# Performance work log

Measured on AMD Instinct MI355X. Metric: run time of the kernel, lower is better.

## Reference

```python
import math
import jax, jax.numpy as jnp
import numpy as np

B, N, DIM, E, G, TOPK, DEPTH = 64, 512, 128, 16, 32, 4, 1
HID = 4 * DIM
EPS = 1e-8
LAMBDA_INIT = 0.8 - 0.6 * math.exp(-0.3 * DEPTH)


def setup_inputs() -> dict:
    key = jax.random.key(0)
    ks = jax.random.split(key, 16)
    d = {}
    d["x"] = jax.random.normal(ks[0], (B, N, DIM), jnp.float32)
    d["bias"] = jnp.zeros((1,), jnp.float32)
    d["attn_scale"] = jnp.ones((DIM,), jnp.float32)
    d["ffn_scale"] = jnp.ones((DIM,), jnp.float32)
    d["Wr"] = jax.random.normal(ks[1], (DIM, E), jnp.float32) * 0.05
    d["br"] = jnp.zeros((E,), jnp.float32)
    d["E1"] = jax.random.uniform(ks[2], (2, E, N, G), jnp.float32)
    d["E2"] = jax.random.uniform(ks[3], (2, E, G, N), jnp.float32)
    d["lambda_q1"] = jax.random.normal(ks[4], (DIM,), jnp.float32) * 0.1
    d["lambda_k1"] = jax.random.normal(ks[5], (DIM,), jnp.float32) * 0.1
    d["lambda_q2"] = jax.random.normal(ks[6], (DIM,), jnp.float32) * 0.1
    d["lambda_k2"] = jax.random.normal(ks[7], (DIM,), jnp.float32) * 0.1
    d["outer_lambda"] = jnp.log(jnp.asarray(99.0, jnp.float32))
    d["W1"] = jax.random.normal(ks[8], (DIM, HID), jnp.float32) * 0.02
    d["b1"] = jnp.zeros((HID,), jnp.float32)
    d["W2"] = jax.random.normal(ks[9], (DIM, HID), jnp.float32) * 0.02
    d["b2"] = jnp.zeros((HID,), jnp.float32)
    d["W3"] = jax.random.normal(ks[10], (HID, DIM), jnp.float32) * 0.02
    d["b3"] = jnp.zeros((DIM,), jnp.float32)
    return d


def _rmsnorm(v, scale):
    # RMSNorm with p<0: full L2 norm over last dim, rms = ||v|| / sqrt(d)
    rms = jnp.linalg.norm(v, axis=-1, keepdims=True) * (DIM ** -0.5)
    return scale * (v / (rms + EPS))


def reference(x, bias, attn_scale, ffn_scale, Wr, br, E1, E2,
              lambda_q1, lambda_k1, lambda_q2, lambda_k2, outer_lambda,
              W1, b1, W2, b2, W3, b3):
    # ---- pre-norm ----
    xn = _rmsnorm(x, attn_scale)                       # [B,N,F]

    # ---- top-k routing (selector) ----
    route_logits = xn @ Wr + br                        # [B,N,E]
    gate = jax.nn.sigmoid(route_logits)
    _, topk_idx = jax.lax.top_k(gate + bias, TOPK)     # [B,N,K]
    mask = jnp.sum(jax.nn.one_hot(topk_idx, E, dtype=gate.dtype), axis=-2)  # [B,N,E]
    # sigmoid(route + log(mask)) == sigmoid(route) * mask (mask in {0,1})
    gated = gate * mask
    route = gated / jnp.sum(gated, axis=-1, keepdims=True)

    # ---- coefficient: concat([1], -(exp(q1.k1) - exp(q2.k2) + lambda_init)) ----
    l1 = jnp.exp(jnp.sum(lambda_q1 * lambda_k1))
    l2 = jnp.exp(jnp.sum(lambda_q2 * lambda_k2))
    lambda_full = -(l1 - l2 + LAMBDA_INIT)
    coef = jnp.concatenate([jnp.ones((1,), x.dtype), lambda_full[None]])  # [2]

    # ---- outer mixing matrix (convex comb of eye with itself -> eye, kept faithful) ----
    w = jax.nn.sigmoid(outer_lambda)
    eye = jnp.eye(DIM, dtype=x.dtype)
    outer = w * eye + (1.0 - w) * eye                  # [F,F]

    # ---- expert graph mixing: bik,e,ekid,ekdj,bjf,fc->bic ----
    A1 = jax.nn.softmax(E1, axis=-1)                   # [2,E,N,G]
    A2 = jax.nn.softmax(E2, axis=-1)                   # [2,E,G,N]
    M = jnp.einsum('ekid,ekdj->ekij', A1, A2)          # [2,E,N,N]
    s = jnp.einsum('bik,ekij->beij', route, M)         # [B,2,N,N]
    xc = jnp.einsum('bjf,fc->bjc', xn, outer)          # [B,N,F]
    attn = jnp.einsum('e,beij,bjc->bic', coef, s, xc)  # [B,N,F]

    x = x + attn

    # ---- SwiGLU FFN (dropout is identity at inference) ----
    xn2 = _rmsnorm(x, ffn_scale)
    h = jax.nn.silu(xn2 @ W1 + b1) * (xn2 @ W2 + b2)   # [B,N,4F]
    x = x + h @ W3 + b3
    return x, topk_idx
```

## Files before the change

### kernel.cpp

```cpp
#include <hip/hip_runtime.h>
#include <math.h>

#define B_ 64
#define N_ 512
#define DIM_ 128
#define E_ 16
#define G_ 32
#define TOPK_ 4
#define HID_ 512

constexpr int BN_ROWS = B_ * N_;

using bf16x8 = __attribute__((ext_vector_type(8))) short;
using s16x4  = __attribute__((ext_vector_type(4))) short;
using f32x4  = __attribute__((ext_vector_type(4))) float;

__device__ __forceinline__ float bf2f(short s) {
    union { unsigned u; float f; } x;
    x.u = ((unsigned)(unsigned short)s) << 16;
    return x.f;
}
__device__ __forceinline__ short f2bf(float f) {
    union { float f; unsigned u; } x;
    x.f = f;
    unsigned r = x.u + 0x7FFF + ((x.u >> 16) & 1);
    return (short)(r >> 16);
}

__device__ __forceinline__ bf16x8 frag_ld(const short* base, int row, int ks, int lhi) {
    int addr = row * 128 + (((ks * 64) + lhi * 16) ^ ((row & 7) << 4));
    return *(const bf16x8*)((const char*)base + addr);
}
__device__ __forceinline__ bf16x8 frag_ld128(const short* base, int row, int ks, int lhi) {
    int addr = row * 256 + (((ks * 64) + lhi * 16) ^ ((row & 7) << 4));
    return *(const bf16x8*)((const char*)base + addr);
}

typedef __attribute__((address_space(3))) void lds_vt;
typedef __attribute__((address_space(1))) const void gbl_vt;
__device__ __forceinline__ void gl2lds(const void* g, void* l) {
    __builtin_amdgcn_global_load_lds((gbl_vt*)g, (lds_vt*)l, 16, 0, 0);
}
#define WAIT_VMCNT(N) do { asm volatile("s_waitcnt vmcnt(" #N ")" ::: "memory"); \
    __builtin_amdgcn_sched_barrier(0); } while (0)
__device__ __forceinline__ void barrier_() {
    __builtin_amdgcn_sched_barrier(0);
    __builtin_amdgcn_s_barrier();
    __builtin_amdgcn_sched_barrier(0);
}
__device__ __forceinline__ void lgkm0_bar() {
    asm volatile("s_waitcnt lgkmcnt(0)" ::: "memory");
    __builtin_amdgcn_sched_barrier(0);
    __builtin_amdgcn_s_barrier();
    __builtin_amdgcn_sched_barrier(0);
}

constexpr int NPRE = BN_ROWS / 4;
constexpr int NXNT = B_ * 16;
constexpr int NSMG = 32 * 512 / 8;
constexpr int NSMN = 1024 / 4;
constexpr int NTW  = 64 * 3;
constexpr int NMISC = NPRE + NXNT + NSMG + NSMN + NTW + 1;

__global__ __launch_bounds__(256) void k_misc(
    const float* __restrict__ x, const float* __restrict__ attn_s,
    const float* __restrict__ Wr, const float* __restrict__ br, const float* __restrict__ bias,
    float* __restrict__ route, float* __restrict__ topk_out,
    short* __restrict__ xnT,
    const float* __restrict__ E1, short* __restrict__ A1nb,
    const float* __restrict__ E2, short* __restrict__ A2nb,
    const float* __restrict__ W1, const float* __restrict__ W2, const float* __restrict__ W3,
    short* __restrict__ W1T, short* __restrict__ W2T, short* __restrict__ W3T,
    const float* __restrict__ lq1, const float* __restrict__ lk1,
    const float* __restrict__ lq2, const float* __restrict__ lk2,
    float lam_init, float* __restrict__ lam_out) {
    __shared__ float tb[32][129];
    __shared__ float invb[32];
    __shared__ float tw[32][33];
    int blk = blockIdx.x;
    int tid = threadIdx.x;

    if (blk < NPRE) {
        int w = tid >> 6, lane = tid & 63;
        int row = blk * 4 + w;
        float2 v = ((const float2*)(x + (size_t)row * DIM_))[lane];
        float ss = v.x * v.x + v.y * v.y;
        for (int off = 32; off; off >>= 1) ss += __shfl_xor(ss, off);
        float inv = 1.0f / (sqrtf(ss * (1.0f / DIM_)) + 1e-8f);
        float2 s = ((const float2*)attn_s)[lane];
        float xn0 = v.x * inv * s.x;
        float xn1 = v.y * inv * s.y;
        int e = lane & 15, chunk = lane >> 4;
        float acc = 0.f;
#pragma unroll
        for (int j = 0; j < 16; ++j) {
            int srcl = chunk * 16 + j;
            float a0 = __shfl(xn0, srcl);
            float a1 = __shfl(xn1, srcl);
            int d0 = chunk * 32 + 2 * j;
            acc += a0 * Wr[d0 * E_ + e] + a1 * Wr[(d0 + 1) * E_ + e];
        }
        acc += __shfl_xor(acc, 16);
        acc += __shfl_xor(acc, 32);
        float gate = 1.0f / (1.0f + expf(-(acc + br[e])));
        float vv = gate + bias[0];
        int rank = 0;
#pragma unroll
        for (int i = 0; i < 16; ++i) {
            float vi = __shfl(vv, i);
            rank += ((vi > vv) || (vi == vv && i < e)) ? 1 : 0;
        }
        bool selq = (rank < TOPK_) && (lane < 16);
        float contrib = selq ? gate : 0.f;
        float ssum = contrib;
        ssum += __shfl_xor(ssum, 1); ssum += __shfl_xor(ssum, 2);
        ssum += __shfl_xor(ssum, 4); ssum += __shfl_xor(ssum, 8);
        if (lane < 16) route[(size_t)row * E_ + e] = selq ? gate / ssum : 0.0f;
        if (selq) topk_out[(size_t)row * TOPK_ + rank] = (float)e;
        return;
    }
    blk -= NPRE;

    if (blk < NXNT) {
        int b = blk >> 4, j0 = (blk & 15) * 32;
        const float* src = x + (size_t)(b * 512 + j0) * 128;
        int r = tid >> 3, c8 = tid & 7;
#pragma unroll
        for (int it = 0; it < 4; ++it) {
            int c4 = c8 + it * 8;
            float4 w4 = *(const float4*)(src + (size_t)r * 128 + c4 * 4);
            tb[r][c4 * 4 + 0] = w4.x; tb[r][c4 * 4 + 1] = w4.y;
            tb[r][c4 * 4 + 2] = w4.z; tb[r][c4 * 4 + 3] = w4.w;
        }
        __syncthreads();
        int sg = tid & 7;
        float ps = 0.f;
#pragma unroll
        for (int j = 0; j < 16; ++j) { float e2 = tb[r][sg * 16 + j]; ps += e2 * e2; }
        ps += __shfl_xor(ps, 1); ps += __shfl_xor(ps, 2); ps += __shfl_xor(ps, 4);
        if (sg == 0) invb[r] = 1.0f / (sqrtf(ps * (1.0f / DIM_)) + 1e-8f);
        __syncthreads();
        int c = tid >> 1, half = tid & 1;
        float sc = attn_s[c];
        short ov[16];
#pragma unroll
        for (int j = 0; j < 16; ++j) {
            int jj = half * 16 + j;
            ov[j] = f2bf(tb[jj][c] * invb[jj] * sc);
        }
        short* dst = xnT + (size_t)(b * 128 + c) * 512 + j0 + half * 16;
        *(bf16x8*)dst = *(bf16x8*)ov;
        *(bf16x8*)(dst + 8) = *(bf16x8*)(ov + 8);
        return;
    }
    blk -= NXNT;

    if (blk < NSMG) {
        int row = blk * 8 + (tid >> 5);
        int l = tid & 31;
        float v = E1[(size_t)row * 32 + l];
        float m = v;
        for (int off = 16; off; off >>= 1) m = fmaxf(m, __shfl_xor(m, off));
        float ev = expf(v - m);
        float s = ev;
        for (int off = 16; off; off >>= 1) s += __shfl_xor(s, off);
        A1nb[(size_t)row * 32 + l] = f2bf(ev / s);
        return;
    }
    blk -= NSMG;

    if (blk < NSMN) {
        int row = blk * 4 + (tid >> 6);
        int l = tid & 63;
        const float* p = E2 + (size_t)row * 512;
        float v[8];
        float m = -1e30f;
#pragma unroll
        for (int j = 0; j < 8; ++j) { v[j] = p[l + j * 64]; m = fmaxf(m, v[j]); }
        for (int off = 32; off; off >>= 1) m = fmaxf(m, __shfl_xor(m, off));
        float s = 0.f;
#pragma unroll
        for (int j = 0; j < 8; ++j) { v[j] = expf(v[j] - m); s += v[j]; }
        for (int off = 32; off; off >>= 1) s += __shfl_xor(s, off);
        float inv = 1.0f / s;
        short* q = A2nb + (size_t)row * 512;
#pragma unroll
        for (int j = 0; j < 8; ++j) q[l + j * 64] = f2bf(v[j] * inv);
        return;
    }
    blk -= NSMN;

    if (blk < NTW) {
        int m = blk >> 6, tile = blk & 63;
        const float* S = (m == 0) ? W1 : (m == 1) ? W2 : W3;
        short* D = (m == 0) ? W1T : (m == 1) ? W2T : W3T;
        int R = (m == 2) ? 512 : 128, C = (m == 2) ? 128 : 512;
        int ctiles = C / 32;
        int r0 = (tile / ctiles) * 32, c0 = (tile % ctiles) * 32;
        int tx = tid & 31, ty = tid >> 5;
#pragma unroll
        for (int r = 0; r < 4; ++r) tw[ty * 4 + r][tx] = S[(size_t)(r0 + ty * 4 + r) * C + c0 + tx];
        __syncthreads();
#pragma unroll
        for (int r = 0; r < 4; ++r) D[(size_t)(c0 + ty * 4 + r) * R + r0 + tx] = f2bf(tw[tx][ty * 4 + r]);
        return;
    }

    if (tid < 64) {
        int l = tid;
        float s1 = lq1[l] * lk1[l] + lq1[l + 64] * lk1[l + 64];
        float s2 = lq2[l] * lk2[l] + lq2[l + 64] * lk2[l + 64];
        for (int off = 32; off; off >>= 1) {
            s1 += __shfl_xor(s1, off);
            s2 += __shfl_xor(s2, off);
        }
        if (l == 0) lam_out[0] = -(expf(s1) - expf(s2) + lam_init);
    }
}

__global__ __launch_bounds__(256) void k_gemm_y(const short* __restrict__ A2nb,
                                                const short* __restrict__ xnT,
                                                short* __restrict__ YT) {
    alignas(16) __shared__ short As0[128 * 64];
    alignas(16) __shared__ short Bs0[128 * 64];
    alignas(16) __shared__ short As1[128 * 64];
    alignas(16) __shared__ short Bs1[128 * 64];
    int id = blockIdx.x;
    int nid = ((id & 7) << 6) + (id >> 3);
    int m0 = (nid & 3) * 128;
    int be = nid >> 2, b = be >> 1, e = be & 1;
    int tid = threadIdx.x, lane = tid & 63, wid = tid >> 6;
    int l15 = lane & 15, lhi = lane >> 4;
    int wr = wid >> 1, wc = wid & 1;
    const short* Asrc = A2nb + (size_t)e * 512 * 512 + (size_t)m0 * 512;
    const short* Bsrc = xnT + (size_t)b * 128 * 512;
    int row8 = lane >> 3;
    int chunk8 = (lane & 7) ^ row8;

    auto stage = [&](short* Ad, short* Bd, int k0) {
#pragma unroll
        for (int t = 0; t < 4; ++t) {
            int i = wid * 4 + t;
            int row = i * 8 + row8;
            gl2lds(Asrc + (size_t)row * 512 + k0 + chunk8 * 8, (char*)Ad + i * 1024);
            gl2lds(Bsrc + (size_t)row * 512 + k0 + chunk8 * 8, (char*)Bd + i * 1024);
        }
    };
    f32x4 acc[4][4] = {};
    stage(As0, Bs0, 0);
    for (int s = 0; s < 8; ++s) {
        const short* Ac = (s & 1) ? As1 : As0;
        const short* Bc = (s & 1) ? Bs1 : Bs0;
        if (s < 7) {
            stage((s & 1) ? As0 : As1, (s & 1) ? Bs0 : Bs1, (s + 1) * 64);
            WAIT_VMCNT(8);
        } else {
            WAIT_VMCNT(0);
        }
        barrier_();
#pragma unroll
        for (int ks = 0; ks < 2; ++ks) {
            bf16x8 af[4], bfr[4];
#pragma unroll
            for (int i = 0; i < 4; ++i) af[i] = frag_ld(Ac, wr * 64 + i * 16 + l15, ks, lhi);
#pragma unroll
            for (int j = 0; j < 4; ++j) bfr[j] = frag_ld(Bc, wc * 64 + j * 16 + l15, ks, lhi);
#pragma unroll
            for (int i = 0; i < 4; ++i)
#pragma unroll
                for (int j = 0; j < 4; ++j)
                    acc[i][j] = __builtin_amdgcn_mfma_f32_16x16x32_bf16(af[i], bfr[j], acc[i][j], 0, 0, 0);
        }
        barrier_();
    }
    short* Yb = YT + (size_t)b * 128 * 1024 + e * 512;
#pragma unroll
    for (int i = 0; i < 4; ++i) {
        int mbase = m0 + wr * 64 + i * 16 + lhi * 4;
#pragma unroll
        for (int j = 0; j < 4; ++j) {
            int n = wc * 64 + j * 16 + l15;
            s16x4 o;
#pragma unroll
            for (int q = 0; q < 4; ++q) o[q] = f2bf(acc[i][j][q]);
            *(s16x4*)(Yb + (size_t)n * 1024 + mbase) = o;
        }
    }
}

__global__ __launch_bounds__(256) void k_attn(const short* __restrict__ A1nb,
                                              const float* __restrict__ route,
                                              const short* __restrict__ YT,
                                              const float* __restrict__ x,
                                              const float* __restrict__ lam_p,
                                              const float* __restrict__ ffn_s,
                                              float* __restrict__ x1,
                                              short* __restrict__ xn2b) {
    alignas(16) __shared__ short Ab0[64 * 64];
    alignas(16) __shared__ short Ab1[64 * 64];
    alignas(16) __shared__ short Bb0[128 * 64];
    alignas(16) __shared__ short Bb1[128 * 64];
    __shared__ float ssbuf[2][64];
    int id = blockIdx.x;
    int nid = ((id & 7) << 6) + (id >> 3);
    int m0 = (nid & 7) * 64;
    int b = nid >> 3;
    float lam = lam_p[0];
    int tid = threadIdx.x, lane = tid & 63, wid = tid >> 6;
    int l15 = lane & 15, lhi = lane >> 4;
    int wr = wid >> 1, wc = wid & 1;
    const short* YTb = YT + (size_t)b * 128 * 1024;
    int row8 = lane >> 3;
    int chunk8 = (lane & 7) ^ row8;

    auto stageB = [&](short* Bd, int k0) {
#pragma unroll
        for (int t = 0; t < 4; ++t) {
            int i = wid * 4 + t;
            int row = i * 8 + row8;
            gl2lds(YTb + (size_t)row * 1024 + k0 + chunk8 * 8, (char*)Bd + i * 1024);
        }
    };
    auto loadA = [&](float (&rv)[2], bf16x8 (&ar)[2], int sn) {
#pragma unroll
        for (int r = 0; r < 2; ++r) {
            int idx = tid + r * 256, rowl = idx >> 3, slot = idx & 7;
            int t = sn * 2 + (slot >> 2);
            int gi = m0 + rowl;
            rv[r] = route[((size_t)b * 512 + gi) * 16 + (t & 15)] * (t >= 16 ? lam : 1.0f);
            ar[r] = *(const bf16x8*)(A1nb + ((size_t)t * 512 + gi) * 32 + (slot & 3) * 8);
        }
    };
    auto writeA = [&](short* dst, float (&rv)[2], bf16x8 (&ar)[2]) {
#pragma unroll
        for (int r = 0; r < 2; ++r) {
            int idx = tid + r * 256, rowl = idx >> 3, slot = idx & 7;
            bf16x8 o;
#pragma unroll
            for (int q = 0; q < 8; ++q) o[q] = f2bf(bf2f(ar[r][q]) * rv[r]);
            *(bf16x8*)((char*)dst + rowl * 128 + ((slot * 16) ^ ((rowl & 7) << 4))) = o;
        }
    };
    f32x4 acc[2][4] = {};
    auto compute = [&](const short* Ac, const short* Bc) {
#pragma unroll
        for (int ks = 0; ks < 2; ++ks) {
            bf16x8 af[2], bfr[4];
#pragma unroll
            for (int i = 0; i < 2; ++i) af[i] = frag_ld(Ac, wr * 32 + i * 16 + l15, ks, lhi);
#pragma unroll
            for (int j = 0; j < 4; ++j) bfr[j] = frag_ld(Bc, wc * 64 + j * 16 + l15, ks, lhi);
#pragma unroll
            for (int i = 0; i < 2; ++i)
#pragma unroll
                for (int j = 0; j < 4; ++j)
                    acc[i][j] = __builtin_amdgcn_mfma_f32_16x16x32_bf16(af[i], bfr[j], acc[i][j], 0, 0, 0);
        }
    };

    float rv0[2], rv1[2];
    bf16x8 ar0[2], ar1[2];
    stageB(Bb0, 0);
    loadA(rv0, ar0, 0);
    for (int sp = 0; sp < 8; ++sp) {
        int s = sp * 2;
        stageB(Bb1, (s + 1) * 64);
        loadA(rv1, ar1, s + 1);
        WAIT_VMCNT(8);
        barrier_();
        writeA(Ab0, rv0, ar0);
        lgkm0_bar();
        compute(Ab0, Bb0);
        barrier_();
        if (s + 2 < 16) {
            stageB(Bb0, (s + 2) * 64);
            loadA(rv0, ar0, s + 2);
            WAIT_VMCNT(8);
        } else {
            WAIT_VMCNT(0);
        }
        barrier_();
        writeA(Ab1, rv1, ar1);
        lgkm0_bar();
        compute(Ab1, Bb1);
        barrier_();
    }
    float x1v[2][4][4];
    float pss[2][4] = {};
#pragma unroll
    for (int i = 0; i < 2; ++i) {
        int gibase = m0 + wr * 32 + i * 16 + lhi * 4;
#pragma unroll
        for (int j = 0; j < 4; ++j) {
            int n = wc * 64 + j * 16 + l15;
#pragma unroll
            for (int q = 0; q < 4; ++q) {
                size_t off = ((size_t)b * 512 + gibase + q) * 128 + n;
                float val = acc[i][j][q] + x[off];
                x1[off] = val;
                x1v[i][j][q] = val;
                pss[i][q] += val * val;
            }
        }
    }
#pragma unroll
    for (int i = 0; i < 2; ++i)
#pragma unroll
        for (int q = 0; q < 4; ++q) {
            float p = pss[i][q];
            p += __shfl_xor(p, 1); p += __shfl_xor(p, 2);
            p += __shfl_xor(p, 4); p += __shfl_xor(p, 8);
            pss[i][q] = p;
        }
    if (l15 == 0) {
#pragma unroll
        for (int i = 0; i < 2; ++i)
#pragma unroll
            for (int q = 0; q < 4; ++q)
                ssbuf[wc][wr * 32 + i * 16 + lhi * 4 + q] = pss[i][q];
    }
    __syncthreads();
#pragma unroll
    for (int i = 0; i < 2; ++i)
#pragma unroll
        for (int q = 0; q < 4; ++q) {
            int rowl = wr * 32 + i * 16 + lhi * 4 + q;
            float ssum = ssbuf[0][rowl] + ssbuf[1][rowl];
            float inv = 1.0f / (sqrtf(ssum * (1.0f / DIM_)) + 1e-8f);
#pragma unroll
            for (int j = 0; j < 4; ++j) {
                int n = wc * 64 + j * 16 + l15;
                xn2b[((size_t)b * 512 + m0 + rowl) * 128 + n] = f2bf(x1v[i][j][q] * inv * ffn_s[n]);
            }
        }
}

__global__ __launch_bounds__(256) void k_ffn(const short* __restrict__ xn2b,
                                             const short* __restrict__ W1T, const float* __restrict__ b1,
                                             const short* __restrict__ W2T, const float* __restrict__ b2,
                                             const short* __restrict__ W3T, const float* __restrict__ b3,
                                             const float* __restrict__ x1,
                                             float* __restrict__ out) {
    alignas(16) __shared__ short Xs[64 * 128];
    alignas(16) __shared__ short Hs[64 * 64];
    alignas(16) __shared__ short W1s[64 * 128];
    alignas(16) __shared__ short W2s[64 * 128];
    alignas(16) __shared__ short W3s[128 * 64];
    int id = blockIdx.x;
    int nid = ((id & 7) << 6) + (id >> 3);
    int m0 = nid * 64;
    int tid = threadIdx.x, lane = tid & 63, wid = tid >> 6;
    int l15 = lane & 15, lhi = lane >> 4;
    int wr = wid >> 1, wc = wid & 1;

    int r4 = lane >> 4;
    int c16 = lane & 15;
    int r8 = lane >> 3;
    int c8 = lane & 7;

    auto stageX = [&]() {
#pragma unroll
        for (int t = 0; t < 4; ++t) {
            int i = wid * 4 + t;
            int row = i * 4 + r4;
            int cs = c16 ^ (row & 7);
            gl2lds(xn2b + (size_t)(m0 + row) * 128 + cs * 8, (char*)Xs + i * 1024);
        }
    };
    auto stageW12 = [&](int p) {
        int n0 = p * 64;
#pragma unroll
        for (int t = 0; t < 8; ++t) {
            int i = wid * 8 + t;
            int which = i >> 4;
            int ii = i & 15;
            int row = ii * 4 + r4;
            int cs = c16 ^ (row & 7);
            const short* S = which ? W2T : W1T;
            short* D = which ? (short*)W2s : (short*)W1s;
            gl2lds(S + (size_t)(n0 + row) * 128 + cs * 8, (char*)D + ii * 1024);
        }
    };
    auto stageW3 = [&](int p) {
        int n0 = p * 64;
#pragma unroll
        for (int t = 0; t < 4; ++t) {
            int i = wid * 4 + t;
            int row = i * 8 + r8;
            int cs = c8 ^ (row & 7);
            gl2lds(W3T + (size_t)row * 512 + n0 + cs * 8, (char*)W3s + i * 1024);
        }
    };

    f32x4 aout[2][4] = {};
    stageX();
    stageW12(0);
    stageW3(0);
    WAIT_VMCNT(0);
    barrier_();
    for (int p = 0; p < 8; ++p) {
        f32x4 a1[2][2] = {}, a2[2][2] = {};
#pragma unroll
        for (int ks = 0; ks < 4; ++ks) {
            bf16x8 af[2], b1f[2], b2f[2];
#pragma unroll
            for (int i = 0; i < 2; ++i) af[i] = frag_ld128(Xs, wr * 32 + i * 16 + l15, ks, lhi);
#pragma unroll
            for (int j = 0; j < 2; ++j) {
                b1f[j] = frag_ld128(W1s, wc * 32 + j * 16 + l15, ks, lhi);
                b2f[j] = frag_ld128(W2s, wc * 32 + j * 16 + l15, ks, lhi);
            }
#pragma unroll
            for (int i = 0; i < 2; ++i)
#pragma unroll
                for (int j = 0; j < 2; ++j) {
                    a1[i][j] = __builtin_amdgcn_mfma_f32_16x16x32_bf16(af[i], b1f[j], a1[i][j], 0, 0, 0);
                    a2[i][j] = __builtin_amdgcn_mfma_f32_16x16x32_bf16(af[i], b2f[j], a2[i][j], 0, 0, 0);
                }
        }
        int nn0 = p * 64;
#pragma unroll
        for (int i = 0; i < 2; ++i) {
            int mloc = wr * 32 + i * 16 + lhi * 4;
#pragma unroll
            for (int j = 0; j < 2; ++j) {
                int nloc = wc * 32 + j * 16 + l15;
                float bb1 = b1[nn0 + nloc], bb2 = b2[nn0 + nloc];
#pragma unroll
                for (int q = 0; q < 4; ++q) {
                    float u = a1[i][j][q] + bb1;
                    float w2v = a2[i][j][q] + bb2;
                    float hv = u / (1.0f + expf(-u)) * w2v;
                    int mq = mloc + q;
                    *(short*)((char*)Hs + mq * 128 + ((nloc * 2) ^ ((mq & 7) << 4))) = f2bf(hv);
                }
            }
        }
        lgkm0_bar();
        if (p < 7) stageW12(p + 1);
#pragma unroll
        for (int ks = 0; ks < 2; ++ks) {
            bf16x8 af[2], bfr[4];
#pragma unroll
            for (int i = 0; i < 2; ++i) af[i] = frag_ld(Hs, wr * 32 + i * 16 + l15, ks, lhi);
#pragma unroll
            for (int j = 0; j < 4; ++j) bfr[j] = frag_ld(W3s, wc * 64 + j * 16 + l15, ks, lhi);
#pragma unroll
            for (int i = 0; i < 2; ++i)
#pragma unroll
                for (int j = 0; j < 4; ++j)
                    aout[i][j] = __builtin_amdgcn_mfma_f32_16x16x32_bf16(af[i], bfr[j], aout[i][j], 0, 0, 0);
        }
        barrier_();
        if (p < 7) {
            stageW3(p + 1);
            WAIT_VMCNT(0);
            barrier_();
        }
    }
#pragma unroll
    for (int i = 0; i < 2; ++i) {
        int mbase = m0 + wr * 32 + i * 16 + lhi * 4;
#pragma unroll
        for (int j = 0; j < 4; ++j) {
            int n = wc * 64 + j * 16 + l15;
            float bv = b3[n];
#pragma unroll
            for (int q = 0; q < 4; ++q) {
                size_t off = (size_t)(mbase + q) * 128 + n;
                out[off] = aout[i][j][q] + x1[off] + bv;
            }
        }
    }
}

constexpr size_t ALIGN_UP(size_t x) { return (x + 255) & ~(size_t)255; }
constexpr size_t SZ_X1   = ALIGN_UP((size_t)BN_ROWS * DIM_ * 4);
constexpr size_t SZ_RT   = ALIGN_UP((size_t)BN_ROWS * E_ * 4);
constexpr size_t SZ_A1   = ALIGN_UP((size_t)32 * 512 * 32 * 2);
constexpr size_t SZ_A2   = ALIGN_UP((size_t)2 * 512 * 512 * 2);
constexpr size_t SZ_XNT  = ALIGN_UP((size_t)B_ * 128 * 512 * 2);
constexpr size_t SZ_YT   = ALIGN_UP((size_t)B_ * 128 * 1024 * 2);
constexpr size_t SZ_XN2B = ALIGN_UP((size_t)BN_ROWS * DIM_ * 2);
constexpr size_t SZ_WT   = ALIGN_UP((size_t)128 * 512 * 2);

extern "C" void kernel_launch(void* const* d_in, const int* in_sizes, int n_in,
                              void* d_out, int out_size, void* d_ws, size_t ws_size,
                              hipStream_t stream) {
    const float* x      = (const float*)d_in[0];
    const float* bias   = (const float*)d_in[1];
    const float* attn_s = (const float*)d_in[2];
    const float* ffn_s  = (const float*)d_in[3];
    const float* Wr     = (const float*)d_in[4];
    const float* br     = (const float*)d_in[5];
    const float* E1     = (const float*)d_in[6];
    const float* E2     = (const float*)d_in[7];
    const float* lq1    = (const float*)d_in[8];
    const float* lk1    = (const float*)d_in[9];
    const float* lq2    = (const float*)d_in[10];
    const float* lk2    = (const float*)d_in[11];
    const float* W1     = (const float*)d_in[13];
    const float* b1     = (const float*)d_in[14];
    const float* W2     = (const float*)d_in[15];
    const float* b2     = (const float*)d_in[16];
    const float* W3     = (const float*)d_in[17];
    const float* b3     = (const float*)d_in[18];

    char* p = (char*)d_ws;
    float* x1   = (float*)p;            p += SZ_X1;
    float* rt   = (float*)p;            p += SZ_RT;
    short* A1nb = (short*)p;            p += SZ_A1;
    short* A2nb = (short*)p;            p += SZ_A2;
    short* xnT  = (short*)p;            p += SZ_XNT;
    short* YT   = (short*)p;            p += SZ_YT;
    short* xn2b = (short*)p;            p += SZ_XN2B;
    short* W1T  = (short*)p;            p += SZ_WT;
    short* W2T  = (short*)p;            p += SZ_WT;
    short* W3T  = (short*)p;            p += SZ_WT;
    float* lam  = (float*)p;            p += 256;

    float* out_x   = (float*)d_out;
    float* out_idx = out_x + (size_t)BN_ROWS * DIM_;

    float lam_init = 0.8f - 0.6f * expf(-0.3f);

    hipLaunchKernelGGL(k_misc, dim3(NMISC), dim3(256), 0, stream,
                       x, attn_s, Wr, br, bias, rt, out_idx, xnT,
                       E1, A1nb, E2, A2nb, W1, W2, W3, W1T, W2T, W3T,
                       lq1, lk1, lq2, lk2, lam_init, lam);
    hipLaunchKernelGGL(k_gemm_y, dim3(512), dim3(256), 0, stream, A2nb, xnT, YT);
    hipLaunchKernelGGL(k_attn, dim3(512), dim3(256), 0, stream, A1nb, rt, YT, x, lam, ffn_s, x1, xn2b);
    hipLaunchKernelGGL(k_ffn, dim3(512), dim3(256), 0, stream, xn2b, W1T, b1, W2T, b2, W3T, b3, x1, out_x);
}
```

Measured before the change: 197.1 us.

## Fuse attention epilogue with SwiGLU FFN and merge routing into transpose blocks

Merges k_attn and k_ffn into one kernel. The residual x1 stays in registers, and the normalized xn2 is written straight into a swizzled LDS tile, so the fp32 x1 and bf16 xn2b global round trips and one launch go away. The routing/top-k computation moves into the xnT transpose blocks, which already hold the x tile in shared memory, so the separate per-row routing blocks and their second read of x are removed. In exchange the fused kernel aliases a 72KB LDS buffer across its phases, which may lower occupancy. It also prefetches W tiles early, before the norm phase.

```diff
diff --git a/kernel.cpp b/kernel.cpp
--- a/kernel.cpp
+++ b/kernel.cpp
@@ -55,12 +55,11 @@
     __builtin_amdgcn_sched_barrier(0);
 }
 
-constexpr int NPRE = BN_ROWS / 4;
 constexpr int NXNT = B_ * 16;
 constexpr int NSMG = 32 * 512 / 8;
 constexpr int NSMN = 1024 / 4;
 constexpr int NTW  = 64 * 3;
-constexpr int NMISC = NPRE + NXNT + NSMG + NSMN + NTW + 1;
+constexpr int NMISC = NXNT + NSMG + NSMN + NTW + 1;
 
 __global__ __launch_bounds__(256) void k_misc(
     const float* __restrict__ x, const float* __restrict__ attn_s,
@@ -74,52 +73,12 @@
     const float* __restrict__ lq1, const float* __restrict__ lk1,
     const float* __restrict__ lq2, const float* __restrict__ lk2,
     float lam_init, float* __restrict__ lam_out) {
-    __shared__ float tb[32][129];
+    __shared__ float tb[32][132];
     __shared__ float invb[32];
+    __shared__ float gbuf[32][17];
     __shared__ float tw[32][33];
     int blk = blockIdx.x;
     int tid = threadIdx.x;
-
-    if (blk < NPRE) {
-        int w = tid >> 6, lane = tid & 63;
-        int row = blk * 4 + w;
-        float2 v = ((const float2*)(x + (size_t)row * DIM_))[lane];
-        float ss = v.x * v.x + v.y * v.y;
-        for (int off = 32; off; off >>= 1) ss += __shfl_xor(ss, off);
-        float inv = 1.0f / (sqrtf(ss * (1.0f / DIM_)) + 1e-8f);
-        float2 s = ((const float2*)attn_s)[lane];
-        float xn0 = v.x * inv * s.x;
-        float xn1 = v.y * inv * s.y;
-        int e = lane & 15, chunk = lane >> 4;
-        float acc = 0.f;
-#pragma unroll
-        for (int j = 0; j < 16; ++j) {
-            int srcl = chunk * 16 + j;
-            float a0 = __shfl(xn0, srcl);
-            float a1 = __shfl(xn1, srcl);
-            int d0 = chunk * 32 + 2 * j;
-            acc += a0 * Wr[d0 * E_ + e] + a1 * Wr[(d0 + 1) * E_ + e];
-        }
-        acc += __shfl_xor(acc, 16);
-        acc += __shfl_xor(acc, 32);
-        float gate = 1.0f / (1.0f + expf(-(acc + br[e])));
-        float vv = gate + bias[0];
-        int rank = 0;
-#pragma unroll
-        for (int i = 0; i < 16; ++i) {
-            float vi = __shfl(vv, i);
-            rank += ((vi > vv) || (vi == vv && i < e)) ? 1 : 0;
-        }
-        bool selq = (rank < TOPK_) && (lane < 16);
-        float contrib = selq ? gate : 0.f;
-        float ssum = contrib;
-        ssum += __shfl_xor(ssum, 1); ssum += __shfl_xor(ssum, 2);
-        ssum += __shfl_xor(ssum, 4); ssum += __shfl_xor(ssum, 8);
-        if (lane < 16) route[(size_t)row * E_ + e] = selq ? gate / ssum : 0.0f;
-        if (selq) topk_out[(size_t)row * TOPK_ + rank] = (float)e;
-        return;
-    }
-    blk -= NPRE;
 
     if (blk < NXNT) {
         int b = blk >> 4, j0 = (blk & 15) * 32;
@@ -140,6 +99,48 @@
         ps += __shfl_xor(ps, 1); ps += __shfl_xor(ps, 2); ps += __shfl_xor(ps, 4);
         if (sg == 0) invb[r] = 1.0f / (sqrtf(ps * (1.0f / DIM_)) + 1e-8f);
         __syncthreads();
+        {
+            int eb = tid & 7;
+            float invr = invb[r];
+            float g0 = 0.f, g1 = 0.f;
+#pragma unroll 4
+            for (int d4 = 0; d4 < 32; ++d4) {
+                float4 tv = *(const float4*)&tb[r][d4 * 4];
+                float4 sv = *(const float4*)(attn_s + d4 * 4);
+                float x0 = tv.x * sv.x, x1v = tv.y * sv.y, x2 = tv.z * sv.z, x3 = tv.w * sv.w;
+                int d0 = d4 * 4;
+                g0 += x0 * Wr[(d0 + 0) * 16 + eb] + x1v * Wr[(d0 + 1) * 16 + eb]
+                    + x2 * Wr[(d0 + 2) * 16 + eb] + x3 * Wr[(d0 + 3) * 16 + eb];
+                g1 += x0 * Wr[(d0 + 0) * 16 + eb + 8] + x1v * Wr[(d0 + 1) * 16 + eb + 8]
+                    + x2 * Wr[(d0 + 2) * 16 + eb + 8] + x3 * Wr[(d0 + 3) * 16 + eb + 8];
+            }
+            float gate0 = 1.0f / (1.0f + expf(-(g0 * invr + br[eb])));
+            float gate1 = 1.0f / (1.0f + expf(-(g1 * invr + br[eb + 8])));
+            gbuf[r][eb] = gate0;
+            gbuf[r][eb + 8] = gate1;
+        }
+        __syncthreads();
+        {
+            int eb = tid & 7;
+            float bv = bias[0];
+            float gate0 = gbuf[r][eb], gate1 = gbuf[r][eb + 8];
+            float v0 = gate0 + bv, v1 = gate1 + bv;
+            int rank0 = 0, rank1 = 0;
+#pragma unroll
+            for (int i = 0; i < 16; ++i) {
+                float vi = gbuf[r][i] + bv;
+                rank0 += ((vi > v0) || (vi == v0 && i < eb)) ? 1 : 0;
+                rank1 += ((vi > v1) || (vi == v1 && i < eb + 8)) ? 1 : 0;
+            }
+            bool s0 = rank0 < TOPK_, s1 = rank1 < TOPK_;
+            float s = (s0 ? gate0 : 0.f) + (s1 ? gate1 : 0.f);
+            s += __shfl_xor(s, 1); s += __shfl_xor(s, 2); s += __shfl_xor(s, 4);
+            size_t grow = (size_t)b * 512 + j0 + r;
+            route[grow * 16 + eb]     = s0 ? gate0 / s : 0.f;
+            route[grow * 16 + eb + 8] = s1 ? gate1 / s : 0.f;
+            if (s0) topk_out[grow * 4 + rank0] = (float)eb;
+            if (s1) topk_out[grow * 4 + rank1] = (float)(eb + 8);
+        }
         int c = tid >> 1, half = tid & 1;
         float sc = attn_s[c];
         short ov[16];
@@ -288,19 +289,26 @@
     }
 }
 
-__global__ __launch_bounds__(256) void k_attn(const short* __restrict__ A1nb,
-                                              const float* __restrict__ route,
-                                              const short* __restrict__ YT,
-                                              const float* __restrict__ x,
-                                              const float* __restrict__ lam_p,
-                                              const float* __restrict__ ffn_s,
-                                              float* __restrict__ x1,
-                                              short* __restrict__ xn2b) {
-    alignas(16) __shared__ short Ab0[64 * 64];
-    alignas(16) __shared__ short Ab1[64 * 64];
-    alignas(16) __shared__ short Bb0[128 * 64];
-    alignas(16) __shared__ short Bb1[128 * 64];
-    __shared__ float ssbuf[2][64];
+__global__ __launch_bounds__(256) void k_attn_ffn(
+    const short* __restrict__ A1nb, const float* __restrict__ route,
+    const short* __restrict__ YT, const float* __restrict__ x,
+    const float* __restrict__ lam_p, const float* __restrict__ ffn_s,
+    const short* __restrict__ W1T, const float* __restrict__ b1,
+    const short* __restrict__ W2T, const float* __restrict__ b2,
+    const short* __restrict__ W3T, const float* __restrict__ b3,
+    float* __restrict__ out) {
+    alignas(16) __shared__ char L[73728];
+    short* Xs    = (short*)L;
+    short* Hs    = (short*)(L + 16384);
+    float* ssbuf = (float*)(L + 16384);
+    short* W1s   = (short*)(L + 24576);
+    short* W2s   = (short*)(L + 40960);
+    short* W3s   = (short*)(L + 57344);
+    short* Ab0 = (short*)(L + 16384);
+    short* Ab1 = (short*)(L + 24576);
+    short* Bb0 = (short*)(L + 32768);
+    short* Bb1 = (short*)(L + 49152);
+
     int id = blockIdx.x;
     int nid = ((id & 7) << 6) + (id >> 3);
     int m0 = (nid & 7) * 64;
@@ -312,6 +320,7 @@
     const short* YTb = YT + (size_t)b * 128 * 1024;
     int row8 = lane >> 3;
     int chunk8 = (lane & 7) ^ row8;
+    int r4 = lane >> 4, c16 = lane & 15;
 
     auto stageB = [&](short* Bd, int k0) {
 #pragma unroll
@@ -385,6 +394,33 @@
         compute(Ab1, Bb1);
         barrier_();
     }
+
+    auto stageW12 = [&](int p) {
+        int n0 = p * 64;
+#pragma unroll
+        for (int t = 0; t < 8; ++t) {
+            int i = wid * 8 + t;
+            int which = i >> 4, ii = i & 15;
+            int row = ii * 4 + r4;
+            int cs = c16 ^ (row & 7);
+            const short* S = which ? W2T : W1T;
+            short* D = which ? (short*)W2s : (short*)W1s;
+            gl2lds(S + (size_t)(n0 + row) * 128 + cs * 8, (char*)D + ii * 1024);
+        }
+    };
+    auto stageW3 = [&](int p) {
+        int n0 = p * 64;
+#pragma unroll
+        for (int t = 0; t < 4; ++t) {
+            int i = wid * 4 + t;
+            int row = i * 8 + row8;
+            int cs = (lane & 7) ^ (row & 7);
+            gl2lds(W3T + (size_t)row * 512 + n0 + cs * 8, (char*)W3s + i * 1024);
+        }
+    };
+    stageW12(0);
+    stageW3(0);
+
     float x1v[2][4][4];
     float pss[2][4] = {};
 #pragma unroll
@@ -397,7 +433,6 @@
             for (int q = 0; q < 4; ++q) {
                 size_t off = ((size_t)b * 512 + gibase + q) * 128 + n;
                 float val = acc[i][j][q] + x[off];
-                x1[off] = val;
                 x1v[i][j][q] = val;
                 pss[i][q] += val * val;
             }
@@ -417,87 +452,29 @@
         for (int i = 0; i < 2; ++i)
 #pragma unroll
             for (int q = 0; q < 4; ++q)
-                ssbuf[wc][wr * 32 + i * 16 + lhi * 4 + q] = pss[i][q];
-    }
-    __syncthreads();
+                ssbuf[wc * 64 + wr * 32 + i * 16 + lhi * 4 + q] = pss[i][q];
+    }
+    lgkm0_bar();
 #pragma unroll
     for (int i = 0; i < 2; ++i)
 #pragma unroll
         for (int q = 0; q < 4; ++q) {
             int rowl = wr * 32 + i * 16 + lhi * 4 + q;
-            float ssum = ssbuf[0][rowl] + ssbuf[1][rowl];
+            float ssum = ssbuf[rowl] + ssbuf[64 + rowl];
             float inv = 1.0f / (sqrtf(ssum * (1.0f / DIM_)) + 1e-8f);
 #pragma unroll
             for (int j = 0; j < 4; ++j) {
                 int n = wc * 64 + j * 16 + l15;
-                xn2b[((size_t)b * 512 + m0 + rowl) * 128 + n] = f2bf(x1v[i][j][q] * inv * ffn_s[n]);
+                *(short*)((char*)Xs + rowl * 256 + ((n * 2) ^ ((rowl & 7) << 4))) =
+                    f2bf(x1v[i][j][q] * inv * ffn_s[n]);
             }
         }
-}
-
-__global__ __launch_bounds__(256) void k_ffn(const short* __restrict__ xn2b,
-                                             const short* __restrict__ W1T, const float* __restrict__ b1,
-                                             const short* __restrict__ W2T, const float* __restrict__ b2,
-                                             const short* __restrict__ W3T, const float* __restrict__ b3,
-                                             const float* __restrict__ x1,
-                                             float* __restrict__ out) {
-    alignas(16) __shared__ short Xs[64 * 128];
-    alignas(16) __shared__ short Hs[64 * 64];
-    alignas(16) __shared__ short W1s[64 * 128];
-    alignas(16) __shared__ short W2s[64 * 128];
-    alignas(16) __shared__ short W3s[128 * 64];
-    int id = blockIdx.x;
-    int nid = ((id & 7) << 6) + (id >> 3);
-    int m0 = nid * 64;
-    int tid = threadIdx.x, lane = tid & 63, wid = tid >> 6;
-    int l15 = lane & 15, lhi = lane >> 4;
-    int wr = wid >> 1, wc = wid & 1;
-
-    int r4 = lane >> 4;
-    int c16 = lane & 15;
-    int r8 = lane >> 3;
-    int c8 = lane & 7;
-
-    auto stageX = [&]() {
-#pragma unroll
-        for (int t = 0; t < 4; ++t) {
-            int i = wid * 4 + t;
-            int row = i * 4 + r4;
-            int cs = c16 ^ (row & 7);
-            gl2lds(xn2b + (size_t)(m0 + row) * 128 + cs * 8, (char*)Xs + i * 1024);
-        }
-    };
-    auto stageW12 = [&](int p) {
-        int n0 = p * 64;
-#pragma unroll
-        for (int t = 0; t < 8; ++t) {
-            int i = wid * 8 + t;
-            int which = i >> 4;
-            int ii = i & 15;
-            int row = ii * 4 + r4;
-            int cs = c16 ^ (row & 7);
-            const short* S = which ? W2T : W1T;
-            short* D = which ? (short*)W2s : (short*)W1s;
-            gl2lds(S + (size_t)(n0 + row) * 128 + cs * 8, (char*)D + ii * 1024);
-        }
-    };
-    auto stageW3 = [&](int p) {
-        int n0 = p * 64;
-#pragma unroll
-        for (int t = 0; t < 4; ++t) {
-            int i = wid * 4 + t;
-            int row = i * 8 + r8;
-            int cs = c8 ^ (row & 7);
-            gl2lds(W3T + (size_t)row * 512 + n0 + cs * 8, (char*)W3s + i * 1024);
-        }
-    };
+    asm volatile("s_waitcnt vmcnt(0) lgkmcnt(0)" ::: "memory");
+    __builtin_amdgcn_sched_barrier(0);
+    __builtin_amdgcn_s_barrier();
+    __builtin_amdgcn_sched_barrier(0);
 
     f32x4 aout[2][4] = {};
-    stageX();
-    stageW12(0);
-    stageW3(0);
-    WAIT_VMCNT(0);
-    barrier_();
     for (int p = 0; p < 8; ++p) {
         f32x4 a1[2][2] = {}, a2[2][2] = {};
 #pragma unroll
@@ -560,28 +537,26 @@
     }
 #pragma unroll
     for (int i = 0; i < 2; ++i) {
-        int mbase = m0 + wr * 32 + i * 16 + lhi * 4;
+        int gibase = m0 + wr * 32 + i * 16 + lhi * 4;
 #pragma unroll
         for (int j = 0; j < 4; ++j) {
             int n = wc * 64 + j * 16 + l15;
             float bv = b3[n];
 #pragma unroll
             for (int q = 0; q < 4; ++q) {
-                size_t off = (size_t)(mbase + q) * 128 + n;
-                out[off] = aout[i][j][q] + x1[off] + bv;
+                size_t off = ((size_t)b * 512 + gibase + q) * 128 + n;
+                out[off] = aout[i][j][q] + x1v[i][j][q] + bv;
             }
         }
     }
 }
 
 constexpr size_t ALIGN_UP(size_t x) { return (x + 255) & ~(size_t)255; }
-constexpr size_t SZ_X1   = ALIGN_UP((size_t)BN_ROWS * DIM_ * 4);
 constexpr size_t SZ_RT   = ALIGN_UP((size_t)BN_ROWS * E_ * 4);
 constexpr size_t SZ_A1   = ALIGN_UP((size_t)32 * 512 * 32 * 2);
 constexpr size_t SZ_A2   = ALIGN_UP((size_t)2 * 512 * 512 * 2);
 constexpr size_t SZ_XNT  = ALIGN_UP((size_t)B_ * 128 * 512 * 2);
 constexpr size_t SZ_YT   = ALIGN_UP((size_t)B_ * 128 * 1024 * 2);
-constexpr size_t SZ_XN2B = ALIGN_UP((size_t)BN_ROWS * DIM_ * 2);
 constexpr size_t SZ_WT   = ALIGN_UP((size_t)128 * 512 * 2);
 
 extern "C" void kernel_launch(void* const* d_in, const int* in_sizes, int n_in,
@@ -607,13 +582,11 @@
     const float* b3     = (const float*)d_in[18];
 
     char* p = (char*)d_ws;
-    float* x1   = (float*)p;            p += SZ_X1;
     float* rt   = (float*)p;            p += SZ_RT;
     short* A1nb = (short*)p;            p += SZ_A1;
     short* A2nb = (short*)p;            p += SZ_A2;
     short* xnT  = (short*)p;            p += SZ_XNT;
     short* YT   = (short*)p;            p += SZ_YT;
-    short* xn2b = (short*)p;            p += SZ_XN2B;
     short* W1T  = (short*)p;            p += SZ_WT;
     short* W2T  = (short*)p;            p += SZ_WT;
     short* W3T  = (short*)p;            p += SZ_WT;
@@ -629,6 +602,6 @@
                        E1, A1nb, E2, A2nb, W1, W2, W3, W1T, W2T, W3T,
                        lq1, lk1, lq2, lk2, lam_init, lam);
     hipLaunchKernelGGL(k_gemm_y, dim3(512), dim3(256), 0, stream, A2nb, xnT, YT);
-    hipLaunchKernelGGL(k_attn, dim3(512), dim3(256), 0, stream, A1nb, rt, YT, x, lam, ffn_s, x1, xn2b);
-    hipLaunchKernelGGL(k_ffn, dim3(512), dim3(256), 0, stream, xn2b, W1T, b1, W2T, b2, W3T, b3, x1, out_x);
-}
+    hipLaunchKernelGGL(k_attn_ffn, dim3(512), dim3(256), 0, stream,
+                       A1nb, rt, YT, x, lam, ffn_s, W1T, b1, W2T, b2, W3T, b3, out_x);
+}
```

New measurement: 183.2 us. 7.1% less time.
